# Optimization experiments

Measured on AMD Instinct MI355X. Metric: run time of the kernel, lower is better.

Reference implementation:

```python
import jax, jax.numpy as jnp
import numpy as np

BLOCK = 32  # GGUF Q8_0 block size


def setup_inputs() -> dict:
    key = jax.random.key(0)
    k1, k2, k3, k4 = jax.random.split(key, 4)
    O, I = 11008, 4096
    x = jax.random.normal(k1, (32, I), dtype=jnp.float32)
    qweight = jax.random.randint(k2, (O, I), 0, 255, dtype=jnp.int32)
    scales = jax.random.uniform(k3, (O, I // BLOCK), dtype=jnp.float32) * 0.01
    bias = jax.random.normal(k4, (O,), dtype=jnp.float32)
    return {"x": x, "qweight": qweight, "scales": scales, "bias": bias}


def dequantize(qweight, scales):
    # Q8_0-style: signed int8 quants, one fp scale per block of 32 along in-dim.
    O, I = qweight.shape
    q = (qweight.astype(scales.dtype) - 127.0).reshape(O, I // BLOCK, BLOCK)
    w = q * scales[:, :, None]  # [O, nb, BLOCK]
    return w.reshape(O, I)


def reference(x, qweight, scales, bias):
    # On-the-fly dequant fused with F.linear: y = x @ W^T + b
    w = dequantize(qweight, scales)           # [O, I]
    return jnp.einsum('bi,oi->bo', x, w) + bias
```

## Files before the change

kernel.cpp:

```cpp
#include <hip/hip_runtime.h>
#include <hip/hip_bf16.h>


#define O_DIM  11008
#define I_DIM  4096
#define NB     128
#define B_DIM  32
#define NSPLIT 8
#define KT     (I_DIM / NSPLIT)
#define PART_STRIDE (B_DIM * O_DIM)

typedef __attribute__((ext_vector_type(8))) short bf16x8;
typedef __attribute__((ext_vector_type(4))) float f32x4;
typedef __attribute__((ext_vector_type(4))) int   i32x4;

static __device__ __forceinline__ unsigned short f2bf(float f) {
    return __builtin_bit_cast(unsigned short, __float2bfloat16(f));
}

static __device__ __forceinline__ bf16x8 dequant8(const i32x4 qa, const i32x4 qb,
                                                  const float s) {
    const float c = -127.0f * s;
    bf16x8 v;
    v[0] = (short)f2bf(fmaf((float)qa[0], s, c));
    v[1] = (short)f2bf(fmaf((float)qa[1], s, c));
    v[2] = (short)f2bf(fmaf((float)qa[2], s, c));
    v[3] = (short)f2bf(fmaf((float)qa[3], s, c));
    v[4] = (short)f2bf(fmaf((float)qb[0], s, c));
    v[5] = (short)f2bf(fmaf((float)qb[1], s, c));
    v[6] = (short)f2bf(fmaf((float)qb[2], s, c));
    v[7] = (short)f2bf(fmaf((float)qb[3], s, c));
    return v;
}

__global__ __launch_bounds__(256, 3) void gemm_kernel(const float* __restrict__ x,
                                                      const int*   __restrict__ qw,
                                                      const float* __restrict__ scales,
                                                      float*       __restrict__ part) {
    __shared__ unsigned short x_s[B_DIM * KT];

    const int t    = threadIdx.x;
    const int wav  = t >> 6;
    const int lan  = t & 63;
    const int lrow = lan & 15;
    const int lq   = lan >> 4;

    const int split  = blockIdx.x;
    const int k_base = split * KT;
    const int o_row  = blockIdx.y * 64 + wav * 16 + lrow;

    const int* __restrict__ wq = qw + o_row * I_DIM + k_base + lq * 8;

    float sc[16];
    {
        const float4* sp = reinterpret_cast<const float4*>(&scales[o_row * NB + split * 16]);
#pragma unroll
        for (int j = 0; j < 4; ++j) {
            const float4 v = sp[j];
            sc[4 * j + 0] = v.x; sc[4 * j + 1] = v.y;
            sc[4 * j + 2] = v.z; sc[4 * j + 3] = v.w;
        }
    }

    i32x4 wa0, wb0, wc0, wd0, wa1, wb1, wc1, wd1, wa2, wb2, wc2, wd2;

#define LOADW(A, B, C, D, c) {                           \
        const int* wp = wq + (c) * 64;                   \
        A = *reinterpret_cast<const i32x4*>(wp);         \
        B = *reinterpret_cast<const i32x4*>(wp + 4);     \
        C = *reinterpret_cast<const i32x4*>(wp + 32);    \
        D = *reinterpret_cast<const i32x4*>(wp + 36); }

    LOADW(wa0, wb0, wc0, wd0, 0)
    LOADW(wa1, wb1, wc1, wd1, 1)

    {
        const int m  = t >> 3;
        const int k0 = (t & 7) * 64;
        const float4* xv = reinterpret_cast<const float4*>(x + m * I_DIM + k_base + k0);
#pragma unroll
        for (int j = 0; j < 8; ++j) {
            const float4 va = xv[2 * j];
            const float4 vb = xv[2 * j + 1];
            bf16x8 v;
            v[0] = (short)f2bf(va.x); v[1] = (short)f2bf(va.y);
            v[2] = (short)f2bf(va.z); v[3] = (short)f2bf(va.w);
            v[4] = (short)f2bf(vb.x); v[5] = (short)f2bf(vb.y);
            v[6] = (short)f2bf(vb.z); v[7] = (short)f2bf(vb.w);
            const int addr = ((m * KT + k0 + j * 8) * 2) ^ ((m & 7) << 4);
            *reinterpret_cast<bf16x8*>(reinterpret_cast<char*>(x_s) + addr) = v;
        }
    }

    __syncthreads();

    f32x4 acc0 = {0.f, 0.f, 0.f, 0.f};
    f32x4 acc1 = {0.f, 0.f, 0.f, 0.f};
    const int swz = (lrow & 7) << 4;

#define CONSUME(A, B, C, D, c) {                                                              \
        const int kb = (c) * 64 + lq * 8;                                                     \
        const bf16x8 a0 = *reinterpret_cast<const bf16x8*>(                                   \
            reinterpret_cast<const char*>(x_s) + ((( lrow       * KT + kb) * 2) ^ swz));      \
        const bf16x8 a1 = *reinterpret_cast<const bf16x8*>(                                   \
            reinterpret_cast<const char*>(x_s) + ((((lrow + 16) * KT + kb) * 2) ^ swz));      \
        const bf16x8 bA = dequant8(A, B, sc[2 * (c)]);                                        \
        acc0 = __builtin_amdgcn_mfma_f32_16x16x32_bf16(a0, bA, acc0, 0, 0, 0);                \
        acc1 = __builtin_amdgcn_mfma_f32_16x16x32_bf16(a1, bA, acc1, 0, 0, 0);                \
        const bf16x8 a2 = *reinterpret_cast<const bf16x8*>(                                   \
            reinterpret_cast<const char*>(x_s) + ((( lrow       * KT + kb + 32) * 2) ^ swz)); \
        const bf16x8 a3 = *reinterpret_cast<const bf16x8*>(                                   \
            reinterpret_cast<const char*>(x_s) + ((((lrow + 16) * KT + kb + 32) * 2) ^ swz)); \
        const bf16x8 bB = dequant8(C, D, sc[2 * (c) + 1]);                                    \
        acc0 = __builtin_amdgcn_mfma_f32_16x16x32_bf16(a2, bB, acc0, 0, 0, 0);                \
        acc1 = __builtin_amdgcn_mfma_f32_16x16x32_bf16(a3, bB, acc1, 0, 0, 0); }

    LOADW(wa2, wb2, wc2, wd2, 2)
    CONSUME(wa0, wb0, wc0, wd0, 0)
    LOADW(wa0, wb0, wc0, wd0, 3)
    CONSUME(wa1, wb1, wc1, wd1, 1)
    LOADW(wa1, wb1, wc1, wd1, 4)
    CONSUME(wa2, wb2, wc2, wd2, 2)
    LOADW(wa2, wb2, wc2, wd2, 5)
    CONSUME(wa0, wb0, wc0, wd0, 3)
    LOADW(wa0, wb0, wc0, wd0, 6)
    CONSUME(wa1, wb1, wc1, wd1, 4)
    LOADW(wa1, wb1, wc1, wd1, 7)
    CONSUME(wa2, wb2, wc2, wd2, 5)
    CONSUME(wa0, wb0, wc0, wd0, 6)
    CONSUME(wa1, wb1, wc1, wd1, 7)

#undef LOADW
#undef CONSUME

    float* pp = part + split * PART_STRIDE;
#pragma unroll
    for (int r = 0; r < 4; ++r) {
        const int m = lq * 4 + r;
        __builtin_nontemporal_store(acc0[r], &pp[m * O_DIM + o_row]);
        __builtin_nontemporal_store(acc1[r], &pp[(m + 16) * O_DIM + o_row]);
    }
}

__global__ __launch_bounds__(256) void reduce_kernel(const float* __restrict__ part,
                                                     const float* __restrict__ bias,
                                                     float* __restrict__ out) {
    const int idx = blockIdx.x * 256 + threadIdx.x;
    const int m   = idx / (O_DIM / 4);
    const int o4  = idx - m * (O_DIM / 4);

    f32x4 v = *reinterpret_cast<const f32x4*>(&bias[o4 * 4]);
#pragma unroll
    for (int s = 0; s < NSPLIT; ++s) {
        const f32x4 p = __builtin_nontemporal_load(
            reinterpret_cast<const f32x4*>(&part[s * PART_STRIDE + m * O_DIM + o4 * 4]));
        v[0] += p[0]; v[1] += p[1]; v[2] += p[2]; v[3] += p[3];
    }
    *reinterpret_cast<f32x4*>(&out[m * O_DIM + o4 * 4]) = v;
}

extern "C" void kernel_launch(void* const* d_in, const int* in_sizes, int n_in,
                              void* d_out, int out_size, void* d_ws, size_t ws_size,
                              hipStream_t stream) {
    const float* x      = (const float*)d_in[0];
    const int*   qw     = (const int*)d_in[1];
    const float* scales = (const float*)d_in[2];
    const float* bias   = (const float*)d_in[3];
    float*       out    = (float*)d_out;
    float*       part   = (float*)d_ws;

    hipLaunchKernelGGL(gemm_kernel, dim3(NSPLIT, O_DIM / 64), dim3(256), 0, stream,
                       x, qw, scales, part);

    hipLaunchKernelGGL(reduce_kernel, dim3((B_DIM * O_DIM / 4) / 256), dim3(256), 0, stream,
                       part, bias, out);
}
```

Measured before the change: 50.45 us.

## Double K-splits and store fp16 partials transposed with per-column reduction

Doubles the K split count so the GEMM launches twice as many blocks, each doing half the K work, and drops the 3-blocks-per-CU launch bound. Partial sums are packed as fp16 in an [split][o][m] layout, so each lane writes 8-byte vectors instead of scalar floats. The reduce kernel now gives each thread one output column and sums 32 batch rows across all splits. The intent is better GEMM parallelism and latency hiding without growing partial traffic. The costs are fp16 rounding of partials and a reduce grid of only 43 blocks, which may underuse the device.

```diff
diff --git a/kernel.cpp b/kernel.cpp
--- a/kernel.cpp
+++ b/kernel.cpp
@@ -6,16 +6,23 @@
 #define I_DIM  4096
 #define NB     128
 #define B_DIM  32
-#define NSPLIT 8
+#define NSPLIT 16
 #define KT     (I_DIM / NSPLIT)
-#define PART_STRIDE (B_DIM * O_DIM)
+#define PART_STRIDE (O_DIM * B_DIM)
 
 typedef __attribute__((ext_vector_type(8))) short bf16x8;
+typedef __attribute__((ext_vector_type(8))) unsigned short u16x8;
 typedef __attribute__((ext_vector_type(4))) float f32x4;
 typedef __attribute__((ext_vector_type(4))) int   i32x4;
 
 static __device__ __forceinline__ unsigned short f2bf(float f) {
     return __builtin_bit_cast(unsigned short, __float2bfloat16(f));
+}
+
+static __device__ __forceinline__ unsigned int pkf16(float a, float b) {
+    const unsigned short ua = __builtin_bit_cast(unsigned short, (_Float16)a);
+    const unsigned short ub = __builtin_bit_cast(unsigned short, (_Float16)b);
+    return (unsigned int)ua | ((unsigned int)ub << 16);
 }
 
 static __device__ __forceinline__ bf16x8 dequant8(const i32x4 qa, const i32x4 qb,
@@ -33,10 +40,10 @@
     return v;
 }
 
-__global__ __launch_bounds__(256, 3) void gemm_kernel(const float* __restrict__ x,
-                                                      const int*   __restrict__ qw,
-                                                      const float* __restrict__ scales,
-                                                      float*       __restrict__ part) {
+__global__ __launch_bounds__(256) void gemm_kernel(const float* __restrict__ x,
+                                                   const int*   __restrict__ qw,
+                                                   const float* __restrict__ scales,
+                                                   unsigned short* __restrict__ part) {
     __shared__ unsigned short x_s[B_DIM * KT];
 
     const int t    = threadIdx.x;
@@ -51,15 +58,12 @@
 
     const int* __restrict__ wq = qw + o_row * I_DIM + k_base + lq * 8;
 
-    float sc[16];
+    float sc[8];
     {
-        const float4* sp = reinterpret_cast<const float4*>(&scales[o_row * NB + split * 16]);
-#pragma unroll
-        for (int j = 0; j < 4; ++j) {
-            const float4 v = sp[j];
-            sc[4 * j + 0] = v.x; sc[4 * j + 1] = v.y;
-            sc[4 * j + 2] = v.z; sc[4 * j + 3] = v.w;
-        }
+        const float4* sp = reinterpret_cast<const float4*>(&scales[o_row * NB + split * 8]);
+        const float4 s0 = sp[0], s1 = sp[1];
+        sc[0] = s0.x; sc[1] = s0.y; sc[2] = s0.z; sc[3] = s0.w;
+        sc[4] = s1.x; sc[5] = s1.y; sc[6] = s1.z; sc[7] = s1.w;
     }
 
     i32x4 wa0, wb0, wc0, wd0, wa1, wb1, wc1, wd1, wa2, wb2, wc2, wd2;
@@ -76,10 +80,10 @@
 
     {
         const int m  = t >> 3;
-        const int k0 = (t & 7) * 64;
+        const int k0 = (t & 7) * 32;
         const float4* xv = reinterpret_cast<const float4*>(x + m * I_DIM + k_base + k0);
 #pragma unroll
-        for (int j = 0; j < 8; ++j) {
+        for (int j = 0; j < 4; ++j) {
             const float4 va = xv[2 * j];
             const float4 vb = xv[2 * j + 1];
             bf16x8 v;
@@ -119,44 +123,43 @@
     CONSUME(wa0, wb0, wc0, wd0, 0)
     LOADW(wa0, wb0, wc0, wd0, 3)
     CONSUME(wa1, wb1, wc1, wd1, 1)
-    LOADW(wa1, wb1, wc1, wd1, 4)
     CONSUME(wa2, wb2, wc2, wd2, 2)
-    LOADW(wa2, wb2, wc2, wd2, 5)
     CONSUME(wa0, wb0, wc0, wd0, 3)
-    LOADW(wa0, wb0, wc0, wd0, 6)
-    CONSUME(wa1, wb1, wc1, wd1, 4)
-    LOADW(wa1, wb1, wc1, wd1, 7)
-    CONSUME(wa2, wb2, wc2, wd2, 5)
-    CONSUME(wa0, wb0, wc0, wd0, 6)
-    CONSUME(wa1, wb1, wc1, wd1, 7)
 
 #undef LOADW
 #undef CONSUME
 
-    float* pp = part + split * PART_STRIDE;
-#pragma unroll
-    for (int r = 0; r < 4; ++r) {
-        const int m = lq * 4 + r;
-        __builtin_nontemporal_store(acc0[r], &pp[m * O_DIM + o_row]);
-        __builtin_nontemporal_store(acc1[r], &pp[(m + 16) * O_DIM + o_row]);
-    }
+    unsigned short* pp = part + split * PART_STRIDE + o_row * B_DIM;
+    const uint2 v0 = make_uint2(pkf16(acc0[0], acc0[1]), pkf16(acc0[2], acc0[3]));
+    const uint2 v1 = make_uint2(pkf16(acc1[0], acc1[1]), pkf16(acc1[2], acc1[3]));
+    *reinterpret_cast<uint2*>(&pp[lq * 4])      = v0;
+    *reinterpret_cast<uint2*>(&pp[16 + lq * 4]) = v1;
 }
 
-__global__ __launch_bounds__(256) void reduce_kernel(const float* __restrict__ part,
+__global__ __launch_bounds__(256) void reduce_kernel(const unsigned short* __restrict__ part,
                                                      const float* __restrict__ bias,
                                                      float* __restrict__ out) {
-    const int idx = blockIdx.x * 256 + threadIdx.x;
-    const int m   = idx / (O_DIM / 4);
-    const int o4  = idx - m * (O_DIM / 4);
+    const int o = blockIdx.x * 256 + threadIdx.x;
+    float v[B_DIM];
+#pragma unroll
+    for (int m = 0; m < B_DIM; ++m) v[m] = 0.f;
 
-    f32x4 v = *reinterpret_cast<const f32x4*>(&bias[o4 * 4]);
 #pragma unroll
     for (int s = 0; s < NSPLIT; ++s) {
-        const f32x4 p = __builtin_nontemporal_load(
-            reinterpret_cast<const f32x4*>(&part[s * PART_STRIDE + m * O_DIM + o4 * 4]));
-        v[0] += p[0]; v[1] += p[1]; v[2] += p[2]; v[3] += p[3];
+        const unsigned short* ps = part + s * PART_STRIDE + o * B_DIM;
+#pragma unroll
+        for (int g = 0; g < 4; ++g) {
+            const u16x8 p = *reinterpret_cast<const u16x8*>(ps + g * 8);
+#pragma unroll
+            for (int j = 0; j < 8; ++j)
+                v[g * 8 + j] += (float)__builtin_bit_cast(_Float16, (unsigned short)p[j]);
+        }
     }
-    *reinterpret_cast<f32x4*>(&out[m * O_DIM + o4 * 4]) = v;
+
+    const float b = bias[o];
+#pragma unroll
+    for (int m = 0; m < B_DIM; ++m)
+        out[m * O_DIM + o] = v[m] + b;
 }
 
 extern "C" void kernel_launch(void* const* d_in, const int* in_sizes, int n_in,
@@ -167,11 +170,11 @@
     const float* scales = (const float*)d_in[2];
     const float* bias   = (const float*)d_in[3];
     float*       out    = (float*)d_out;
-    float*       part   = (float*)d_ws;
+    unsigned short* part = (unsigned short*)d_ws;
 
     hipLaunchKernelGGL(gemm_kernel, dim3(NSPLIT, O_DIM / 64), dim3(256), 0, stream,
                        x, qw, scales, part);
 
-    hipLaunchKernelGGL(reduce_kernel, dim3((B_DIM * O_DIM / 4) / 256), dim3(256), 0, stream,
+    hipLaunchKernelGGL(reduce_kernel, dim3(O_DIM / 256), dim3(256), 0, stream,
                        part, bias, out);
 }
```

After: 48.07 us. 4.7% less time.
